# Kernel tuning notes

Hardware: AMD Instinct MI355X
Metric: run time of the kernel (lower is better)

## Reference

```python
import jax, jax.numpy as jnp
import numpy as np


def setup_inputs() -> dict:
    key = jax.random.key(0)
    ks = jax.random.split(key, 8)
    B, C, S = 32, 64, 64          # batch, per-atom channels, molecule size
    CC = 128                      # x_concat channels; CC + 2*C == OC
    OC = 256                      # conv block channels
    w = lambda k, shp: jax.random.normal(k, shp, dtype=jnp.float32) * 0.05
    return {
        "x": jax.random.normal(ks[0], (B, C, S), dtype=jnp.float32),
        "xc": jax.random.normal(ks[1], (B, CC, S - 1, S), dtype=jnp.float32),
        "W1": w(ks[2], (OC, OC)), "b1": w(ks[3], (OC,)),
        "W2": w(ks[4], (OC, OC)), "b2": w(ks[5], (OC,)),
        "W3": w(ks[6], (OC, OC)), "b3": w(ks[7], (OC,)),
        "batch_size": B,
        "size": S,
    }


def _conv1x1_relu(h, W, b):
    # 1x1 Conv2d == per-position matmul over channels
    return jax.nn.relu(jnp.einsum('bchw,oc->bohw', h, W) + b[None, :, None, None])


def reference(x, xc, W1, b1, W2, b2, W3, b3, batch_size, size):
    # Build pair matrix: for shift d+1, roll[d, i] = (i - (d+1)) % size
    i = jnp.arange(size)
    d = jnp.arange(1, size)
    idx = (i[None, :] - d[:, None]) % size            # [S-1, S]
    rolled = x[:, :, idx]                              # [B, C, S-1, S] gather
    x_rep = jnp.broadcast_to(x[:, :, None, :], rolled.shape)
    # torch.cat((*x_concat, pair_matrix), dim=1): concat channels then [x_rep, rolled]
    pairs_cat = jnp.concatenate([xc, x_rep, rolled], axis=1)  # [B, OC, S-1, S]
    h = _conv1x1_relu(pairs_cat, W1, b1)
    h = _conv1x1_relu(h, W2, b2)
    h = _conv1x1_relu(h, W3, b3)
    return h
```

## Files before the change

kernel.cpp:

```cpp
#include <hip/hip_runtime.h>
#include <stdint.h>


typedef __attribute__((ext_vector_type(8))) __bf16 bf16x8;
typedef __attribute__((ext_vector_type(4))) float f32x4;
typedef __attribute__((ext_vector_type(4))) unsigned short u16x4;
typedef __attribute__((ext_vector_type(8))) unsigned short u16x8;

__device__ __forceinline__ unsigned short f2bf(float f) {
  unsigned int u = __builtin_bit_cast(unsigned int, f);
  u += 0x7FFFu + ((u >> 16) & 1u);
  return (unsigned short)(u >> 16);
}

__device__ __forceinline__ int xaddr(int pos, int c) {
  int slot = (pos << 3) + ((((c & 63) >> 3) ^ pos) & 7);
  return ((c >> 6) << 13) + (slot << 3) + (c & 7);
}

__global__ void wconv_kernel(const float* __restrict__ W1, const float* __restrict__ W2,
                             const float* __restrict__ W3, unsigned short* __restrict__ wb) {
  int i = (blockIdx.x * 256 + threadIdx.x) * 4;
  const float* Ws[3] = {W1, W2, W3};
#pragma unroll
  for (int L = 0; L < 3; ++L) {
    f32x4 a = *(const f32x4*)(Ws[L] + i);
    u16x4 p;
#pragma unroll
    for (int v = 0; v < 4; ++v) p[v] = f2bf(a[v]);
    *(u16x4*)(wb + L * 65536 + i) = p;
  }
}

__global__ __launch_bounds__(512, 1)
void fused_kernel(const float* __restrict__ x, const float* __restrict__ xc,
                  const unsigned short* __restrict__ wb,
                  const float* __restrict__ b1, const float* __restrict__ b2,
                  const float* __restrict__ b3, float* __restrict__ out) {
  __shared__ __align__(16) unsigned char lraw[65536];
  unsigned short* X = (unsigned short*)lraw;
  float* bounce = (float*)lraw;

  const int r = blockIdx.x;
  const int b0 = r / 63;
  const int dd = r % 63;
  const int d = dd + 1;
  const int tid = threadIdx.x;
  const int lane = tid & 63;
  const int g16 = lane >> 4;
  const int l16 = lane & 15;
  const int wv = tid >> 6;

  const int p = tid & 63;
  const int c0 = (tid >> 6) << 3;

  float xreg[2][8];
#pragma unroll
  for (int rr = 0; rr < 2; ++rr)
#pragma unroll
    for (int j = 0; j < 8; ++j)
      xreg[rr][j] = x[((b0 + 16 * rr) * 64 + c0 + j) * 64 + p];

#pragma unroll
  for (int cr = 0; cr < 4; ++cr) {
    const int rr = cr >> 1;
    const int ck = cr & 1;
    const int b = b0 + 16 * rr;
    u16x8 v;
#pragma unroll
    for (int j = 0; j < 8; ++j)
      v[j] = f2bf(xc[(((b * 128 + ck * 64 + c0 + j) * 63) + dd) * 64 + p]);
    *(u16x8*)&X[xaddr(rr * 64 + p, ck * 64 + c0)] = v;
  }
  __syncthreads();

  for (int layer = 0; layer < 3; ++layer) {
    const unsigned short* wl = wb + layer * 65536;
    const float* bias = (layer == 0) ? b1 : (layer == 1) ? b2 : b3;
    const bool al3 = (layer == 0);

    f32x4 acc[2][8] = {};
    const int ow = wv * 32;

    const int kkmid = al3 ? 4 : 8;

#pragma unroll
    for (int kk = 0; kk < 8; ++kk) {
      if (al3 && kk == 4) {
#pragma unroll
        for (int rr = 0; rr < 2; ++rr) {
          u16x8 v;
#pragma unroll
          for (int j = 0; j < 8; ++j) v[j] = f2bf(xreg[rr][j]);
          *(u16x8*)&X[xaddr(rr * 64 + p, 128 + c0)] = v;
        }
        __syncthreads();
      }
      int kb = kk * 32 + g16 * 8;
      bool a3 = al3 && (kk >= 6);
      int cc = a3 ? (128 + (kb & 63)) : kb;
      bf16x8 afr[2];
#pragma unroll
      for (int mf = 0; mf < 2; ++mf)
        afr[mf] = __builtin_bit_cast(
            bf16x8, *(const u16x8*)(wl + (ow + mf * 16 + l16) * 256 + kb));
      bf16x8 bfr[4];
#pragma unroll
      for (int nf = 0; nf < 4; ++nf) {
        int i = nf * 16 + l16;
        int ie = a3 ? ((i - d) & 63) : i;
        bfr[nf] = __builtin_bit_cast(bf16x8, *(const u16x8*)&X[xaddr(ie, cc)]);
      }
#pragma unroll
      for (int mf = 0; mf < 2; ++mf)
#pragma unroll
        for (int nf = 0; nf < 4; ++nf)
          acc[mf][nf] = __builtin_amdgcn_mfma_f32_16x16x32_bf16(afr[mf], bfr[nf], acc[mf][nf], 0, 0, 0);
#pragma unroll
      for (int nf = 0; nf < 4; ++nf) {
        int i = nf * 16 + l16;
        int ie = 64 + (a3 ? ((i - d) & 63) : i);
        bfr[nf] = __builtin_bit_cast(bf16x8, *(const u16x8*)&X[xaddr(ie, cc)]);
      }
#pragma unroll
      for (int mf = 0; mf < 2; ++mf)
#pragma unroll
        for (int nf = 0; nf < 4; ++nf)
          acc[mf][4 + nf] = __builtin_amdgcn_mfma_f32_16x16x32_bf16(afr[mf], bfr[nf], acc[mf][4 + nf], 0, 0, 0);
    }
    __syncthreads();

    if (layer < 2) {
#pragma unroll
      for (int mf = 0; mf < 2; ++mf) {
        int o0 = ow + mf * 16 + g16 * 4;
        f32x4 bv = *(const f32x4*)(bias + o0);
#pragma unroll
        for (int nf = 0; nf < 8; ++nf) {
          int pos = nf * 16 + l16;
          u16x4 pk;
#pragma unroll
          for (int v = 0; v < 4; ++v)
            pk[v] = f2bf(fmaxf(acc[mf][nf][v] + bv[v], 0.f));
          *(u16x4*)&X[xaddr(pos, o0)] = pk;
        }
      }
      __syncthreads();
    } else {
#pragma unroll
      for (int rr = 0; rr < 2; ++rr) {
#pragma unroll
        for (int mf = 0; mf < 2; ++mf) {
          int oh0 = ow + mf * 16 + g16 * 4;
          f32x4 bv = *(const f32x4*)(bias + oh0);
#pragma unroll
          for (int nq = 0; nq < 4; ++nq) {
            int pos = nq * 16 + l16;
#pragma unroll
            for (int v = 0; v < 4; ++v) {
              int oh = oh0 + v;
              bounce[oh * 64 + (pos ^ ((oh & 7) << 2))] =
                  fmaxf(acc[mf][rr * 4 + nq][v] + bv[v], 0.f);
            }
          }
        }
        __syncthreads();
        int bq = b0 + 16 * rr;
#pragma unroll
        for (int q = 0; q < 8; ++q) {
          int u = q * 512 + tid;
          int oh = u >> 4;
          int pos4 = (u & 15) << 2;
          f32x4 vv = *(const f32x4*)&bounce[oh * 64 + (pos4 ^ ((oh & 7) << 2))];
          *(f32x4*)&out[(((bq * 256 + oh) * 63) + dd) * 64 + pos4] = vv;
        }
        if (rr == 0) __syncthreads();
      }
    }
  }
}

extern "C" void kernel_launch(void* const* d_in, const int* in_sizes, int n_in,
                              void* d_out, int out_size, void* d_ws, size_t ws_size,
                              hipStream_t stream) {
  const float* x  = (const float*)d_in[0];
  const float* xc = (const float*)d_in[1];
  const float* W1 = (const float*)d_in[2];
  const float* b1 = (const float*)d_in[3];
  const float* W2 = (const float*)d_in[4];
  const float* b2 = (const float*)d_in[5];
  const float* W3 = (const float*)d_in[6];
  const float* b3 = (const float*)d_in[7];
  float* out = (float*)d_out;
  unsigned short* wb = (unsigned short*)d_ws;

  wconv_kernel<<<64, 256, 0, stream>>>(W1, W2, W3, wb);
  fused_kernel<<<1008, 512, 0, stream>>>(x, xc, wb, b1, b2, b3, out);
}
```

Baseline: 106.2 us.

## Make blocks persistent over four units and prefetch next unit's inputs

Each block now processes four (batch, shift) units in sequence, with a grid of 252 instead of 1008. While the last layer's epilogue runs, it issues the global loads for the next unit so their latency overlaps the output writes. The LDS bounce staging for the final output is removed and results are written straight to global memory as scalar stores. The x channels are now loaded up front along with xc instead of midway through layer 0. Trade-offs: 252 blocks may not fill the 256 CUs, the prefetch raises register pressure, and the scalar output stores are less coalesced than the old 16-byte ones.

```diff
diff --git a/kernel.cpp b/kernel.cpp
--- a/kernel.cpp
+++ b/kernel.cpp
@@ -39,142 +39,139 @@
                   const float* __restrict__ b3, float* __restrict__ out) {
   __shared__ __align__(16) unsigned char lraw[65536];
   unsigned short* X = (unsigned short*)lraw;
-  float* bounce = (float*)lraw;
 
-  const int r = blockIdx.x;
-  const int b0 = r / 63;
-  const int dd = r % 63;
-  const int d = dd + 1;
   const int tid = threadIdx.x;
   const int lane = tid & 63;
   const int g16 = lane >> 4;
   const int l16 = lane & 15;
   const int wv = tid >> 6;
-
+  const int ow = wv * 32;
   const int p = tid & 63;
   const int c0 = (tid >> 6) << 3;
 
-  float xreg[2][8];
+  const int unit0 = blockIdx.x * 4;
+
+  float xr[6][8];
+  auto ldunit = [&](int u) {
+    int bb = u / 63, de = u % 63;
 #pragma unroll
-  for (int rr = 0; rr < 2; ++rr)
+    for (int cr = 0; cr < 6; ++cr) {
+      int rr = cr / 3, ck = cr - rr * 3;
+      int b = bb + 16 * rr;
 #pragma unroll
-    for (int j = 0; j < 8; ++j)
-      xreg[rr][j] = x[((b0 + 16 * rr) * 64 + c0 + j) * 64 + p];
+      for (int j = 0; j < 8; ++j)
+        xr[cr][j] = (ck < 2) ? xc[(((b * 128 + ck * 64 + c0 + j) * 63) + de) * 64 + p]
+                             : x[(b * 64 + c0 + j) * 64 + p];
+    }
+  };
+  auto wrunit = [&]() {
+#pragma unroll
+    for (int cr = 0; cr < 6; ++cr) {
+      int rr = cr / 3, ck = cr - rr * 3;
+      u16x8 v;
+#pragma unroll
+      for (int j = 0; j < 8; ++j) v[j] = f2bf(xr[cr][j]);
+      *(u16x8*)&X[xaddr(rr * 64 + p, ck * 64 + c0)] = v;
+    }
+  };
+
+  ldunit(unit0);
+  wrunit();
+  __syncthreads();
+
+#pragma unroll 1
+  for (int i = 0; i < 4; ++i) {
+    const int unit = unit0 + i;
+    const int b0 = unit / 63;
+    const int dd = unit % 63;
+    const int d = dd + 1;
+
+#pragma unroll 1
+    for (int layer = 0; layer < 3; ++layer) {
+      const unsigned short* wl = wb + layer * 65536;
+      const float* bias = (layer == 0) ? b1 : (layer == 1) ? b2 : b3;
+      const bool al3 = (layer == 0);
+
+      f32x4 acc[2][8] = {};
 
 #pragma unroll
-  for (int cr = 0; cr < 4; ++cr) {
-    const int rr = cr >> 1;
-    const int ck = cr & 1;
-    const int b = b0 + 16 * rr;
-    u16x8 v;
+      for (int kk = 0; kk < 8; ++kk) {
+        int kb = kk * 32 + g16 * 8;
+        bool a3 = al3 && (kk >= 6);
+        int cc = a3 ? (128 + (kb & 63)) : kb;
+        bf16x8 afr[2];
 #pragma unroll
-    for (int j = 0; j < 8; ++j)
-      v[j] = f2bf(xc[(((b * 128 + ck * 64 + c0 + j) * 63) + dd) * 64 + p]);
-    *(u16x8*)&X[xaddr(rr * 64 + p, ck * 64 + c0)] = v;
-  }
-  __syncthreads();
+        for (int mf = 0; mf < 2; ++mf)
+          afr[mf] = __builtin_bit_cast(
+              bf16x8, *(const u16x8*)(wl + (ow + mf * 16 + l16) * 256 + kb));
+        bf16x8 bfr[4];
+#pragma unroll
+        for (int nf = 0; nf < 4; ++nf) {
+          int ii = nf * 16 + l16;
+          int ie = a3 ? ((ii - d) & 63) : ii;
+          bfr[nf] = __builtin_bit_cast(bf16x8, *(const u16x8*)&X[xaddr(ie, cc)]);
+        }
+#pragma unroll
+        for (int mf = 0; mf < 2; ++mf)
+#pragma unroll
+          for (int nf = 0; nf < 4; ++nf)
+            acc[mf][nf] = __builtin_amdgcn_mfma_f32_16x16x32_bf16(afr[mf], bfr[nf], acc[mf][nf], 0, 0, 0);
+#pragma unroll
+        for (int nf = 0; nf < 4; ++nf) {
+          int ii = nf * 16 + l16;
+          int ie = 64 + (a3 ? ((ii - d) & 63) : ii);
+          bfr[nf] = __builtin_bit_cast(bf16x8, *(const u16x8*)&X[xaddr(ie, cc)]);
+        }
+#pragma unroll
+        for (int mf = 0; mf < 2; ++mf)
+#pragma unroll
+          for (int nf = 0; nf < 4; ++nf)
+            acc[mf][4 + nf] = __builtin_amdgcn_mfma_f32_16x16x32_bf16(afr[mf], bfr[nf], acc[mf][4 + nf], 0, 0, 0);
+      }
 
-  for (int layer = 0; layer < 3; ++layer) {
-    const unsigned short* wl = wb + layer * 65536;
-    const float* bias = (layer == 0) ? b1 : (layer == 1) ? b2 : b3;
-    const bool al3 = (layer == 0);
-
-    f32x4 acc[2][8] = {};
-    const int ow = wv * 32;
-
-    const int kkmid = al3 ? 4 : 8;
+      if (layer < 2) {
+        __syncthreads();
+#pragma unroll
+        for (int mf = 0; mf < 2; ++mf) {
+          int o0 = ow + mf * 16 + g16 * 4;
+          f32x4 bv = *(const f32x4*)(bias + o0);
+#pragma unroll
+          for (int nf = 0; nf < 8; ++nf) {
+            int pos = nf * 16 + l16;
+            u16x4 pk;
+#pragma unroll
+            for (int v = 0; v < 4; ++v)
+              pk[v] = f2bf(fmaxf(acc[mf][nf][v] + bv[v], 0.f));
+            *(u16x4*)&X[xaddr(pos, o0)] = pk;
+          }
+        }
+        __syncthreads();
+      } else {
+        if (i < 3) ldunit(unit + 1);
 
 #pragma unroll
-    for (int kk = 0; kk < 8; ++kk) {
-      if (al3 && kk == 4) {
+        for (int rr = 0; rr < 2; ++rr) {
+          const int bq = b0 + 16 * rr;
 #pragma unroll
-        for (int rr = 0; rr < 2; ++rr) {
-          u16x8 v;
+          for (int mf = 0; mf < 2; ++mf) {
+            int o0 = ow + mf * 16 + g16 * 4;
+            f32x4 bv = *(const f32x4*)(bias + o0);
 #pragma unroll
-          for (int j = 0; j < 8; ++j) v[j] = f2bf(xreg[rr][j]);
-          *(u16x8*)&X[xaddr(rr * 64 + p, 128 + c0)] = v;
-        }
-        __syncthreads();
-      }
-      int kb = kk * 32 + g16 * 8;
-      bool a3 = al3 && (kk >= 6);
-      int cc = a3 ? (128 + (kb & 63)) : kb;
-      bf16x8 afr[2];
+            for (int nf = 0; nf < 4; ++nf) {
+              int pos = nf * 16 + l16;
 #pragma unroll
-      for (int mf = 0; mf < 2; ++mf)
-        afr[mf] = __builtin_bit_cast(
-            bf16x8, *(const u16x8*)(wl + (ow + mf * 16 + l16) * 256 + kb));
-      bf16x8 bfr[4];
-#pragma unroll
-      for (int nf = 0; nf < 4; ++nf) {
-        int i = nf * 16 + l16;
-        int ie = a3 ? ((i - d) & 63) : i;
-        bfr[nf] = __builtin_bit_cast(bf16x8, *(const u16x8*)&X[xaddr(ie, cc)]);
-      }
-#pragma unroll
-      for (int mf = 0; mf < 2; ++mf)
-#pragma unroll
-        for (int nf = 0; nf < 4; ++nf)
-          acc[mf][nf] = __builtin_amdgcn_mfma_f32_16x16x32_bf16(afr[mf], bfr[nf], acc[mf][nf], 0, 0, 0);
-#pragma unroll
-      for (int nf = 0; nf < 4; ++nf) {
-        int i = nf * 16 + l16;
-        int ie = 64 + (a3 ? ((i - d) & 63) : i);
-        bfr[nf] = __builtin_bit_cast(bf16x8, *(const u16x8*)&X[xaddr(ie, cc)]);
-      }
-#pragma unroll
-      for (int mf = 0; mf < 2; ++mf)
-#pragma unroll
-        for (int nf = 0; nf < 4; ++nf)
-          acc[mf][4 + nf] = __builtin_amdgcn_mfma_f32_16x16x32_bf16(afr[mf], bfr[nf], acc[mf][4 + nf], 0, 0, 0);
-    }
-    __syncthreads();
-
-    if (layer < 2) {
-#pragma unroll
-      for (int mf = 0; mf < 2; ++mf) {
-        int o0 = ow + mf * 16 + g16 * 4;
-        f32x4 bv = *(const f32x4*)(bias + o0);
-#pragma unroll
-        for (int nf = 0; nf < 8; ++nf) {
-          int pos = nf * 16 + l16;
-          u16x4 pk;
-#pragma unroll
-          for (int v = 0; v < 4; ++v)
-            pk[v] = f2bf(fmaxf(acc[mf][nf][v] + bv[v], 0.f));
-          *(u16x4*)&X[xaddr(pos, o0)] = pk;
-        }
-      }
-      __syncthreads();
-    } else {
-#pragma unroll
-      for (int rr = 0; rr < 2; ++rr) {
-#pragma unroll
-        for (int mf = 0; mf < 2; ++mf) {
-          int oh0 = ow + mf * 16 + g16 * 4;
-          f32x4 bv = *(const f32x4*)(bias + oh0);
-#pragma unroll
-          for (int nq = 0; nq < 4; ++nq) {
-            int pos = nq * 16 + l16;
-#pragma unroll
-            for (int v = 0; v < 4; ++v) {
-              int oh = oh0 + v;
-              bounce[oh * 64 + (pos ^ ((oh & 7) << 2))] =
-                  fmaxf(acc[mf][rr * 4 + nq][v] + bv[v], 0.f);
+              for (int v = 0; v < 4; ++v)
+                out[(((bq * 256 + o0 + v) * 63) + dd) * 64 + pos] =
+                    fmaxf(acc[mf][rr * 4 + nf][v] + bv[v], 0.f);
             }
           }
         }
-        __syncthreads();
-        int bq = b0 + 16 * rr;
-#pragma unroll
-        for (int q = 0; q < 8; ++q) {
-          int u = q * 512 + tid;
-          int oh = u >> 4;
-          int pos4 = (u & 15) << 2;
-          f32x4 vv = *(const f32x4*)&bounce[oh * 64 + (pos4 ^ ((oh & 7) << 2))];
-          *(f32x4*)&out[(((bq * 256 + oh) * 63) + dd) * 64 + pos4] = vv;
+
+        if (i < 3) {
+          __syncthreads();
+          wrunit();
+          __syncthreads();
         }
-        if (rr == 0) __syncthreads();
       }
     }
   }
@@ -195,5 +192,5 @@
   unsigned short* wb = (unsigned short*)d_ws;
 
   wconv_kernel<<<64, 256, 0, stream>>>(W1, W2, W3, wb);
-  fused_kernel<<<1008, 512, 0, stream>>>(x, xc, wb, b1, b2, b3, out);
+  fused_kernel<<<252, 512, 0, stream>>>(x, xc, wb, b1, b2, b3, out);
 }
```

Measured after the change: 199.3 us. 87.8% more time.
